# Performance work log

Measured on AMD Instinct MI355X. Metric: run time of the kernel, lower is better.

The kernel has to match this reference:

```python
import jax, jax.numpy as jnp
import numpy as np
from itertools import product

DIM = 384
HEADS = 8
DIM_HEAD = 64
INNER = HEADS * DIM_HEAD  # 512
KS = 3                    # kernel_size (attention window)
PAD = KS // 2
W_WIN = KS * KS           # 9
SCALE = DIM_HEAD ** -0.5


def setup_inputs() -> dict:
    key = jax.random.key(0)
    k1, k2, k3, k4, k5 = jax.random.split(key, 5)
    B, H, W = 4, 56, 56
    x = jax.random.normal(k1, (B, DIM, H, W), dtype=jnp.float32)
    # 1x1 conv weights stored as (out_ch, in_ch)
    Wq = jax.random.normal(k2, (INNER, DIM), dtype=jnp.float32) * (DIM ** -0.5)
    Wkv = jax.random.normal(k3, (2 * INNER, DIM), dtype=jnp.float32) * (DIM ** -0.5)
    Wo = jax.random.normal(k4, (DIM, INNER), dtype=jnp.float32) * (INNER ** -0.5)
    bo = jax.random.normal(k5, (DIM,), dtype=jnp.float32) * 0.01
    return {"x": x, "Wq": Wq, "Wkv": Wkv, "Wo": Wo, "bo": bo}


def _conv1x1(x, w):
    # x: (B,Cin,H,W), w: (Cout,Cin) -> (B,Cout,H,W)
    return jnp.einsum('bchw,oc->bohw', x, w)


def reference(x, Wq, Wkv, Wo, bo):
    B, C, H, W = x.shape
    q = _conv1x1(x, Wq)                       # (B, INNER, H, W)
    kv = _conv1x1(x, Wkv)                     # (B, 2*INNER, H, W)
    k, v = jnp.split(kv, 2, axis=1)
    # split channels heads-major, matching torch reshape (B, heads, dh, H, W)
    q = q.reshape(B, HEADS, DIM_HEAD, H, W)
    k = k.reshape(B, HEADS, DIM_HEAD, H, W)
    v = v.reshape(B, HEADS, DIM_HEAD, H, W)
    # zero-pad spatial dims (matches F.unfold zero padding: padded taps get logit 0)
    k_pad = jnp.pad(k, ((0, 0), (0, 0), (0, 0), (PAD, PAD), (PAD, PAD)))
    v_pad = jnp.pad(v, ((0, 0), (0, 0), (0, 0), (PAD, PAD), (PAD, PAD)))
    offsets = list(product(range(KS), range(KS)))  # row-major = unfold order
    # dots: (B, heads, H, W, w)
    dots = jnp.stack([
        jnp.einsum('bhdxy,bhdxy->bhxy', q, k_pad[:, :, :, i:i + H, j:j + W])
        for (i, j) in offsets
    ], axis=-1) * SCALE
    attn = jax.nn.softmax(dots, axis=-1)      # softmax over the 9-tap window
    # weighted sum of shifted v: (B, heads, dh, H, W)
    out = sum(
        attn[:, :, None, :, :, w_idx] * v_pad[:, :, :, i:i + H, j:j + W]
        for w_idx, (i, j) in enumerate(offsets)
    )
    out = out.reshape(B, INNER, H, W)
    return _conv1x1(out, Wo) + bo[None, :, None, None]
```

## Files before the change

### kernel.cpp

```cpp
#include <hip/hip_runtime.h>


#define HW 3136
#define WIMG 56
#define QKV_CH 1536
#define SCALE 0.125f
#define KSTR 72
#define NROWS 180
#define QKV_T 6422528

typedef __bf16 bf16x8_t __attribute__((ext_vector_type(8)));
typedef float f32x4_t __attribute__((ext_vector_type(4)));
typedef unsigned short ushort8 __attribute__((ext_vector_type(8)));

__device__ __forceinline__ float bf2f(unsigned short u) {
    return __uint_as_float(((unsigned int)u) << 16);
}
__device__ __forceinline__ unsigned short f2bf(float f) {
    unsigned int u = __float_as_uint(f);
    u += 0x7FFFu + ((u >> 16) & 1u);
    return (unsigned short)(u >> 16);
}

__device__ __forceinline__ void gll16(const unsigned short* g, unsigned short* l) {
    __builtin_amdgcn_global_load_lds(
        (const __attribute__((address_space(1))) unsigned int*)g,
        (__attribute__((address_space(3))) unsigned int*)l,
        16, 0, 0);
}

__global__ __launch_bounds__(256) void cvt_all(
    const float* __restrict__ x,
    const float* __restrict__ Wq, const float* __restrict__ Wkv,
    const float* __restrict__ Wo,
    unsigned short* __restrict__ xT,
    unsigned short* __restrict__ wT, unsigned short* __restrict__ wT3)
{
    __shared__ unsigned short Tl[64 * 36];
    const int bx = blockIdx.x;
    const int t = threadIdx.x;

    if (bx < 2400) {
        const int sblk = bx % 50;
        const int kblk = (bx / 50) % 12;
        const int b    = bx / 600;

        if (sblk == 49) {
            unsigned short* dst = xT + (((size_t)b * 25 + 24) * 12 + kblk) * 4096 + 2048;
            *reinterpret_cast<uint4*>(dst + t * 8) = (uint4){0, 0, 0, 0};
            return;
        }

        const float* xp = x + ((size_t)b * 384 + (size_t)kblk * 32) * HW + sblk * 64;
        const int c = t >> 3;
#pragma unroll
        for (int i = 0; i < 2; i++) {
            const int sc = (t & 7) + 8 * i;
            const float4 v = *reinterpret_cast<const float4*>(xp + (size_t)c * HW + sc * 4);
            const int s4 = sc * 4;
            Tl[(s4 + 0) * 36 + c] = f2bf(v.x);
            Tl[(s4 + 1) * 36 + c] = f2bf(v.y);
            Tl[(s4 + 2) * 36 + c] = f2bf(v.z);
            Tl[(s4 + 3) * 36 + c] = f2bf(v.w);
        }
        __syncthreads();

        const int row = t >> 2, gran = t & 3;
        const uint2 lo = *reinterpret_cast<const uint2*>(&Tl[row * 36 + gran * 8]);
        const uint2 hi = *reinterpret_cast<const uint2*>(&Tl[row * 36 + gran * 8 + 4]);
        uint4 o; o.x = lo.x; o.y = lo.y; o.z = hi.x; o.w = hi.y;
        unsigned short* dst = xT + (((size_t)b * 25 + (sblk >> 1)) * 12 + kblk) * 4096
                            + (sblk & 1) * 2048;
        *reinterpret_cast<uint4*>(dst + t * 8) = o;
        return;
    }

    const int i = (bx - 2400) * 256 + t;
    if (i < 73728) {
        const int g = i & 3;
        const int idx3 = i >> 2;
        const int o128 = idx3 & 127;
        const int rest = idx3 >> 7;
        const int kb = rest % 12, oblk = rest / 12;
        const int o = oblk * 128 + o128;
        const int k0 = kb * 32 + g * 8;
        const float* src = (o < 512) ? (Wq + (size_t)o * 384 + k0)
                                     : (Wkv + (size_t)(o - 512) * 384 + k0);
        const float4 v0 = *reinterpret_cast<const float4*>(src);
        const float4 v1 = *reinterpret_cast<const float4*>(src + 4);
        uint4 u;
        u.x = (unsigned int)f2bf(v0.x) | ((unsigned int)f2bf(v0.y) << 16);
        u.y = (unsigned int)f2bf(v0.z) | ((unsigned int)f2bf(v0.w) << 16);
        u.z = (unsigned int)f2bf(v1.x) | ((unsigned int)f2bf(v1.y) << 16);
        u.w = (unsigned int)f2bf(v1.z) | ((unsigned int)f2bf(v1.w) << 16);
        reinterpret_cast<uint4*>(wT)[i] = u;
    } else {
        const int j = i - 73728;
        const int g = j & 3;
        const int idx3 = j >> 2;
        const int o128 = idx3 & 127;
        const int rest = idx3 >> 7;
        const int kb = rest % 16, oblk = rest / 16;
        const int o = oblk * 128 + o128;
        const float* src = Wo + (size_t)o * 512 + kb * 32 + g * 8;
        const float4 v0 = *reinterpret_cast<const float4*>(src);
        const float4 v1 = *reinterpret_cast<const float4*>(src + 4);
        uint4 u;
        u.x = (unsigned int)f2bf(v0.x) | ((unsigned int)f2bf(v0.y) << 16);
        u.y = (unsigned int)f2bf(v0.z) | ((unsigned int)f2bf(v0.w) << 16);
        u.z = (unsigned int)f2bf(v1.x) | ((unsigned int)f2bf(v1.y) << 16);
        u.w = (unsigned int)f2bf(v1.z) | ((unsigned int)f2bf(v1.w) << 16);
        reinterpret_cast<uint4*>(wT3)[j] = u;
    }
}

__global__ __launch_bounds__(256) void gemm1(
    const unsigned short* __restrict__ xT,
    const unsigned short* __restrict__ wT,
    unsigned short* __restrict__ qkvT)
{
    __shared__ __align__(16) unsigned short A_lds[128 * 32];
    __shared__ __align__(16) unsigned short B_lds[128 * 32];

    const int sblk = blockIdx.x;
    const int oblk = blockIdx.y;
    const int b  = blockIdx.z;
    const int t  = threadIdx.x;
    const int lane = t & 63, w = t >> 6;
    const int quad = lane >> 4, mrow = lane & 15;
    const int wm = w >> 1, wn = w & 1;

    const unsigned short* wsrc = wT + ((size_t)oblk * 12) * 4096;
    const unsigned short* xsrc = xT + (((size_t)b * 25 + sblk) * 12) * 4096;

    f32x4_t acc[4][4];
#pragma unroll
    for (int m = 0; m < 4; m++)
#pragma unroll
        for (int n = 0; n < 4; n++) acc[m][n] = (f32x4_t){0.f, 0.f, 0.f, 0.f};

    for (int kb = 0; kb < 12; kb++) {
        __syncthreads();
        gll16(wsrc + (size_t)kb * 4096 + t * 8,        A_lds + t * 8);
        gll16(wsrc + (size_t)kb * 4096 + 2048 + t * 8, A_lds + 2048 + t * 8);
        gll16(xsrc + (size_t)kb * 4096 + t * 8,        B_lds + t * 8);
        gll16(xsrc + (size_t)kb * 4096 + 2048 + t * 8, B_lds + 2048 + t * 8);
        __syncthreads();

        bf16x8_t af[4], bf[4];
#pragma unroll
        for (int m = 0; m < 4; m++)
            af[m] = *reinterpret_cast<const bf16x8_t*>(&A_lds[(wm * 64 + m * 16 + mrow) * 32 + quad * 8]);
#pragma unroll
        for (int n = 0; n < 4; n++)
            bf[n] = *reinterpret_cast<const bf16x8_t*>(&B_lds[(wn * 64 + n * 16 + mrow) * 32 + quad * 8]);
#pragma unroll
        for (int m = 0; m < 4; m++)
#pragma unroll
            for (int n = 0; n < 4; n++)
                acc[m][n] = __builtin_amdgcn_mfma_f32_16x16x32_bf16(af[m], bf[n], acc[m][n], 0, 0, 0);
    }

    const int which = oblk >> 2;
    const int hq = (oblk & 3) * 2 + wm;
    const int s0 = sblk * 128 + wn * 64;
    unsigned short* outb = qkvT + (size_t)which * QKV_T
                         + ((size_t)(b * 8 + hq) * HW) * 64;
#pragma unroll
    for (int m = 0; m < 4; m++) {
        const int d0 = m * 16 + quad * 4;
#pragma unroll
        for (int n = 0; n < 4; n++) {
            const int ss = s0 + n * 16 + mrow;
            if (ss < HW) {
                uint2 u;
                u.x = (unsigned int)f2bf(acc[m][n][0]) | ((unsigned int)f2bf(acc[m][n][1]) << 16);
                u.y = (unsigned int)f2bf(acc[m][n][2]) | ((unsigned int)f2bf(acc[m][n][3]) << 16);
                *reinterpret_cast<uint2*>(outb + (size_t)ss * 64 + d0) = u;
            }
        }
    }
}

__global__ __launch_bounds__(256) void natt2(
    const unsigned short* __restrict__ qkvT,
    unsigned short* __restrict__ aoT)
{
    __shared__ __align__(16) unsigned short smem[2 * NROWS * KSTR];
    unsigned short* Kl = smem;
    unsigned short* Vl = smem + NROWS * KSTR;
    float* dred = reinterpret_cast<float*>(smem);

    const int t = threadIdx.x, lane = t & 63, w = t >> 6;
    const int sblk = blockIdx.x;
    const int s0 = sblk * 64;
    const int s  = s0 + lane;
    const int h  = blockIdx.y, b = blockIdx.z;
    const int y  = s / WIMG, xx = s % WIMG;

    const unsigned short* qg = qkvT + ((size_t)(b * 8 + h) * HW) * 64;
    const unsigned short* kg = qg + (size_t)QKV_T;
    const unsigned short* vg = qg + (size_t)(2 * QKV_T);

#pragma unroll
    for (int i = 0; i < 6; i++) {
        const int f = i * 256 + t;
        if (f < NROWS * 8) {
            const int row = f >> 3, c8 = f & 7;
            int srow = s0 - 59 + row;
            srow = min(max(srow, 0), HW - 1);
            const uint4 k4 = *reinterpret_cast<const uint4*>(kg + (size_t)srow * 64 + c8 * 8);
            const uint4 v4 = *reinterpret_cast<const uint4*>(vg + (size_t)srow * 64 + c8 * 8);
            *reinterpret_cast<uint4*>(&Kl[row * KSTR + c8 * 8]) = k4;
            *reinterpret_cast<uint4*>(&Vl[row * KSTR + c8 * 8]) = v4;
        }
    }

    int   roff[9];
    float msk[9];
#pragma unroll
    for (int ty = 0; ty < 3; ty++)
#pragma unroll
        for (int tx = 0; tx < 3; tx++) {
            const int tap = ty * 3 + tx;
            const int ny = y + ty - 1, nx = xx + tx - 1;
            const bool v = (ny >= 0) && (ny < WIMG) && (nx >= 0) && (nx < WIMG);
            roff[tap] = (v ? ((ty - 1) * WIMG + (tx - 1)) : 0) * KSTR;
            msk[tap]  = v ? 1.f : 0.f;
        }

    float qv[16];
    {
        const uint4 q0 = *reinterpret_cast<const uint4*>(qg + (size_t)s * 64 + w * 16);
        const uint4 q1 = *reinterpret_cast<const uint4*>(qg + (size_t)s * 64 + w * 16 + 8);
        qv[0] = bf2f((unsigned short)(q0.x & 0xffff)); qv[1] = bf2f((unsigned short)(q0.x >> 16));
        qv[2] = bf2f((unsigned short)(q0.y & 0xffff)); qv[3] = bf2f((unsigned short)(q0.y >> 16));
        qv[4] = bf2f((unsigned short)(q0.z & 0xffff)); qv[5] = bf2f((unsigned short)(q0.z >> 16));
        qv[6] = bf2f((unsigned short)(q0.w & 0xffff)); qv[7] = bf2f((unsigned short)(q0.w >> 16));
        qv[8]  = bf2f((unsigned short)(q1.x & 0xffff)); qv[9]  = bf2f((unsigned short)(q1.x >> 16));
        qv[10] = bf2f((unsigned short)(q1.y & 0xffff)); qv[11] = bf2f((unsigned short)(q1.y >> 16));
        qv[12] = bf2f((unsigned short)(q1.z & 0xffff)); qv[13] = bf2f((unsigned short)(q1.z >> 16));
        qv[14] = bf2f((unsigned short)(q1.w & 0xffff)); qv[15] = bf2f((unsigned short)(q1.w >> 16));
    }

    __syncthreads();

    const int rbase = (59 + lane) * KSTR + w * 16;

    float dots[9];
#pragma unroll
    for (int tp = 0; tp < 9; tp++) dots[tp] = 0.f;
#pragma unroll
    for (int hh = 0; hh < 2; hh++) {
#pragma unroll
        for (int tp = 0; tp < 9; tp++) {
            const ushort8 kk = *reinterpret_cast<const ushort8*>(&Kl[rbase + roff[tp] + hh * 8]);
#pragma unroll
            for (int j = 0; j < 8; j++)
                dots[tp] += qv[hh * 8 + j] * bf2f(kk[j]);
        }
    }

    __syncthreads();
#pragma unroll
    for (int tp = 0; tp < 9; tp++) dred[(tp * 4 + w) * 64 + lane] = dots[tp];
    __syncthreads();

    float mx = -1e30f, dt[9];
#pragma unroll
    for (int tp = 0; tp < 9; tp++) {
        const float sum = dred[(tp * 4 + 0) * 64 + lane] + dred[(tp * 4 + 1) * 64 + lane] +
                          dred[(tp * 4 + 2) * 64 + lane] + dred[(tp * 4 + 3) * 64 + lane];
        dt[tp] = msk[tp] * (sum * SCALE);
        mx = fmaxf(mx, dt[tp]);
    }
    float se = 0.f, w9[9];
#pragma unroll
    for (int tp = 0; tp < 9; tp++) { w9[tp] = __expf(dt[tp] - mx); se += w9[tp]; }
    const float inv = 1.f / se;
#pragma unroll
    for (int tp = 0; tp < 9; tp++) w9[tp] *= inv * msk[tp];

    float o[16];
#pragma unroll
    for (int dd = 0; dd < 16; dd++) o[dd] = 0.f;
#pragma unroll
    for (int hh = 0; hh < 2; hh++) {
        ushort8 vfr[9];
#pragma unroll
        for (int tp = 0; tp < 9; tp++)
            vfr[tp] = *reinterpret_cast<const ushort8*>(&Vl[rbase + roff[tp] + hh * 8]);
#pragma unroll
        for (int j = 0; j < 8; j++)
#pragma unroll
            for (int tp = 0; tp < 9; tp++)
                o[hh * 8 + j] += w9[tp] * bf2f(vfr[tp][j]);
    }

    __align__(16) unsigned short ov[16];
#pragma unroll
    for (int dd = 0; dd < 16; dd++) ov[dd] = f2bf(o[dd]);

    unsigned short* dst = aoT + (((size_t)(b * 49 + sblk)) * 16 + (h * 2 + (w >> 1))) * 2048
                        + lane * 32 + (w & 1) * 16;
    *reinterpret_cast<uint4*>(dst)     = *reinterpret_cast<const uint4*>(ov);
    *reinterpret_cast<uint4*>(dst + 8) = *reinterpret_cast<const uint4*>(ov + 8);
}

__global__ __launch_bounds__(256) void gemm3(
    const unsigned short* __restrict__ aoT,
    const unsigned short* __restrict__ wT3,
    const float* __restrict__ bias,
    float* __restrict__ out)
{
    __shared__ __align__(16) unsigned short A_lds[128 * 32];
    __shared__ __align__(16) unsigned short B_lds[64 * 32];

    const int sblk = blockIdx.x;
    const int oblk = blockIdx.y;
    const int b  = blockIdx.z;
    const int t  = threadIdx.x;
    const int lane = t & 63, w = t >> 6;
    const int quad = lane >> 4, mrow = lane & 15;
    const int wm = w >> 1, wn = w & 1;

    const unsigned short* asrc = wT3 + (size_t)oblk * 16 * 4096;
    const unsigned short* bsrc = aoT + ((size_t)(b * 49 + sblk)) * 16 * 2048;

    f32x4_t acc[4][2];
#pragma unroll
    for (int m = 0; m < 4; m++)
#pragma unroll
        for (int n = 0; n < 2; n++) acc[m][n] = (f32x4_t){0.f, 0.f, 0.f, 0.f};

    for (int kb = 0; kb < 16; kb++) {
        __syncthreads();
        gll16(asrc + (size_t)kb * 4096 + t * 8,        A_lds + t * 8);
        gll16(asrc + (size_t)kb * 4096 + 2048 + t * 8, A_lds + 2048 + t * 8);
        gll16(bsrc + (size_t)kb * 2048 + t * 8,        B_lds + t * 8);
        __syncthreads();

        bf16x8_t af[4], bf[2];
#pragma unroll
        for (int m = 0; m < 4; m++)
            af[m] = *reinterpret_cast<const bf16x8_t*>(&A_lds[(wm * 64 + m * 16 + mrow) * 32 + quad * 8]);
#pragma unroll
        for (int n = 0; n < 2; n++)
            bf[n] = *reinterpret_cast<const bf16x8_t*>(&B_lds[(wn * 32 + n * 16 + mrow) * 32 + quad * 8]);
#pragma unroll
        for (int m = 0; m < 4; m++)
#pragma unroll
            for (int n = 0; n < 2; n++)
                acc[m][n] = __builtin_amdgcn_mfma_f32_16x16x32_bf16(af[m], bf[n], acc[m][n], 0, 0, 0);
    }

    const int o0 = oblk * 128 + wm * 64;
    const int s0 = sblk * 64 + wn * 32;
    float* outb = out + (size_t)b * 384 * HW;
#pragma unroll
    for (int m = 0; m < 4; m++)
#pragma unroll
        for (int n = 0; n < 2; n++) {
            const int ss = s0 + n * 16 + mrow;
#pragma unroll
            for (int r = 0; r < 4; r++) {
                const int oo = o0 + m * 16 + quad * 4 + r;
                outb[(size_t)oo * HW + ss] = acc[m][n][r] + bias[oo];
            }
        }
}

extern "C" void kernel_launch(void* const* d_in, const int* in_sizes, int n_in,
                              void* d_out, int out_size, void* d_ws, size_t ws_size,
                              hipStream_t stream) {
    const float* x   = (const float*)d_in[0];
    const float* Wq  = (const float*)d_in[1];
    const float* Wkv = (const float*)d_in[2];
    const float* Wo  = (const float*)d_in[3];
    const float* bo  = (const float*)d_in[4];
    float* out = (float*)d_out;

    unsigned short* xT   = (unsigned short*)d_ws;
    unsigned short* wT   = xT + (size_t)4915200;
    unsigned short* wT3  = wT + (size_t)589824;
    unsigned short* qkvT = wT3 + (size_t)196608;
    unsigned short* aoT  = qkvT + (size_t)(3 * QKV_T);

    cvt_all<<<dim3(2784), 256, 0, stream>>>(x, Wq, Wkv, Wo, xT, wT, wT3);

    gemm1<<<dim3(25, 12, 4), 256, 0, stream>>>(xT, wT, qkvT);
    natt2<<<dim3(49, 8, 4), 256, 0, stream>>>(qkvT, aoT);
    gemm3<<<dim3(49, 3, 4), 256, 0, stream>>>(aoT, wT3, bo, out);
}
```

Baseline: 143.1 us.

## Widen neighborhood-attention tiles to 128 pixels and reuse one LDS buffer for K then V

Each natt2 block now covers 128 pixels instead of 64, with 2 threads per pixel splitting the head dim into 32-wide halves instead of 4 quarters. This cuts the halo overhead per pixel and the cross-thread dot reduction. K and V share one LDS buffer: V is loaded after the K dot products, which lowers LDS footprint but puts the V load on the critical path. The grid shrinks to 25x8x4 blocks, and the last block is masked at the image boundary.

Measured after the change: 141.1 us. No clear change (-1.4%).

```diff
diff --git a/kernel.cpp b/kernel.cpp
--- a/kernel.cpp
+++ b/kernel.cpp
@@ -6,7 +6,7 @@
 #define QKV_CH 1536
 #define SCALE 0.125f
 #define KSTR 72
-#define NROWS 180
+#define NROWS 242
 #define QKV_T 6422528
 
 typedef __bf16 bf16x8_t __attribute__((ext_vector_type(8)));
@@ -186,33 +186,32 @@
     const unsigned short* __restrict__ qkvT,
     unsigned short* __restrict__ aoT)
 {
-    __shared__ __align__(16) unsigned short smem[2 * NROWS * KSTR];
-    unsigned short* Kl = smem;
-    unsigned short* Vl = smem + NROWS * KSTR;
-    float* dred = reinterpret_cast<float*>(smem);
-
-    const int t = threadIdx.x, lane = t & 63, w = t >> 6;
+    __shared__ __align__(16) unsigned short KV[NROWS * KSTR];
+    __shared__ float dred[9 * 2 * 128];
+
+    const int t = threadIdx.x;
+    const int p  = t & 127;
+    const int dq = t >> 7;
     const int sblk = blockIdx.x;
-    const int s0 = sblk * 64;
-    const int s  = s0 + lane;
+    const int s0 = sblk * 128;
+    const int s  = s0 + p;
     const int h  = blockIdx.y, b = blockIdx.z;
-    const int y  = s / WIMG, xx = s % WIMG;
+    const int sc = min(s, HW - 1);
+    const int y  = sc / WIMG, xx = sc % WIMG;
 
     const unsigned short* qg = qkvT + ((size_t)(b * 8 + h) * HW) * 64;
     const unsigned short* kg = qg + (size_t)QKV_T;
     const unsigned short* vg = qg + (size_t)(2 * QKV_T);
 
 #pragma unroll
-    for (int i = 0; i < 6; i++) {
+    for (int i = 0; i < 8; i++) {
         const int f = i * 256 + t;
         if (f < NROWS * 8) {
             const int row = f >> 3, c8 = f & 7;
-            int srow = s0 - 59 + row;
+            int srow = s0 - 57 + row;
             srow = min(max(srow, 0), HW - 1);
             const uint4 k4 = *reinterpret_cast<const uint4*>(kg + (size_t)srow * 64 + c8 * 8);
-            const uint4 v4 = *reinterpret_cast<const uint4*>(vg + (size_t)srow * 64 + c8 * 8);
-            *reinterpret_cast<uint4*>(&Kl[row * KSTR + c8 * 8]) = k4;
-            *reinterpret_cast<uint4*>(&Vl[row * KSTR + c8 * 8]) = v4;
+            *reinterpret_cast<uint4*>(&KV[row * KSTR + c8 * 8]) = k4;
         }
     }
 
@@ -229,48 +228,56 @@
             msk[tap]  = v ? 1.f : 0.f;
         }
 
-    float qv[16];
-    {
-        const uint4 q0 = *reinterpret_cast<const uint4*>(qg + (size_t)s * 64 + w * 16);
-        const uint4 q1 = *reinterpret_cast<const uint4*>(qg + (size_t)s * 64 + w * 16 + 8);
-        qv[0] = bf2f((unsigned short)(q0.x & 0xffff)); qv[1] = bf2f((unsigned short)(q0.x >> 16));
-        qv[2] = bf2f((unsigned short)(q0.y & 0xffff)); qv[3] = bf2f((unsigned short)(q0.y >> 16));
-        qv[4] = bf2f((unsigned short)(q0.z & 0xffff)); qv[5] = bf2f((unsigned short)(q0.z >> 16));
-        qv[6] = bf2f((unsigned short)(q0.w & 0xffff)); qv[7] = bf2f((unsigned short)(q0.w >> 16));
-        qv[8]  = bf2f((unsigned short)(q1.x & 0xffff)); qv[9]  = bf2f((unsigned short)(q1.x >> 16));
-        qv[10] = bf2f((unsigned short)(q1.y & 0xffff)); qv[11] = bf2f((unsigned short)(q1.y >> 16));
-        qv[12] = bf2f((unsigned short)(q1.z & 0xffff)); qv[13] = bf2f((unsigned short)(q1.z >> 16));
-        qv[14] = bf2f((unsigned short)(q1.w & 0xffff)); qv[15] = bf2f((unsigned short)(q1.w >> 16));
+    float qv[32];
+#pragma unroll
+    for (int c = 0; c < 4; c++) {
+        const uint4 q4 = *reinterpret_cast<const uint4*>(qg + (size_t)sc * 64 + dq * 32 + c * 8);
+        qv[c*8+0] = bf2f((unsigned short)(q4.x & 0xffff)); qv[c*8+1] = bf2f((unsigned short)(q4.x >> 16));
+        qv[c*8+2] = bf2f((unsigned short)(q4.y & 0xffff)); qv[c*8+3] = bf2f((unsigned short)(q4.y >> 16));
+        qv[c*8+4] = bf2f((unsigned short)(q4.z & 0xffff)); qv[c*8+5] = bf2f((unsigned short)(q4.z >> 16));
+        qv[c*8+6] = bf2f((unsigned short)(q4.w & 0xffff)); qv[c*8+7] = bf2f((unsigned short)(q4.w >> 16));
     }
 
     __syncthreads();
 
-    const int rbase = (59 + lane) * KSTR + w * 16;
+    const int rbase = (57 + p) * KSTR + dq * 32;
 
     float dots[9];
 #pragma unroll
     for (int tp = 0; tp < 9; tp++) dots[tp] = 0.f;
 #pragma unroll
-    for (int hh = 0; hh < 2; hh++) {
+    for (int ch = 0; ch < 4; ch++) {
 #pragma unroll
         for (int tp = 0; tp < 9; tp++) {
-            const ushort8 kk = *reinterpret_cast<const ushort8*>(&Kl[rbase + roff[tp] + hh * 8]);
+            const ushort8 kk = *reinterpret_cast<const ushort8*>(&KV[rbase + roff[tp] + ch * 8]);
 #pragma unroll
             for (int j = 0; j < 8; j++)
-                dots[tp] += qv[hh * 8 + j] * bf2f(kk[j]);
+                dots[tp] += qv[ch * 8 + j] * bf2f(kk[j]);
         }
     }
 
     __syncthreads();
-#pragma unroll
-    for (int tp = 0; tp < 9; tp++) dred[(tp * 4 + w) * 64 + lane] = dots[tp];
+
+#pragma unroll
+    for (int tp = 0; tp < 9; tp++) dred[(tp * 2 + dq) * 128 + p] = dots[tp];
+#pragma unroll
+    for (int i = 0; i < 8; i++) {
+        const int f = i * 256 + t;
+        if (f < NROWS * 8) {
+            const int row = f >> 3, c8 = f & 7;
+            int srow = s0 - 57 + row;
+            srow = min(max(srow, 0), HW - 1);
+            const uint4 v4 = *reinterpret_cast<const uint4*>(vg + (size_t)srow * 64 + c8 * 8);
+            *reinterpret_cast<uint4*>(&KV[row * KSTR + c8 * 8]) = v4;
+        }
+    }
+
     __syncthreads();
 
     float mx = -1e30f, dt[9];
 #pragma unroll
     for (int tp = 0; tp < 9; tp++) {
-        const float sum = dred[(tp * 4 + 0) * 64 + lane] + dred[(tp * 4 + 1) * 64 + lane] +
-                          dred[(tp * 4 + 2) * 64 + lane] + dred[(tp * 4 + 3) * 64 + lane];
+        const float sum = dred[(tp * 2 + 0) * 128 + p] + dred[(tp * 2 + 1) * 128 + p];
         dt[tp] = msk[tp] * (sum * SCALE);
         mx = fmaxf(mx, dt[tp]);
     }
@@ -281,30 +288,33 @@
 #pragma unroll
     for (int tp = 0; tp < 9; tp++) w9[tp] *= inv * msk[tp];
 
-    float o[16];
-#pragma unroll
-    for (int dd = 0; dd < 16; dd++) o[dd] = 0.f;
-#pragma unroll
-    for (int hh = 0; hh < 2; hh++) {
+    float o[32];
+#pragma unroll
+    for (int dd = 0; dd < 32; dd++) o[dd] = 0.f;
+#pragma unroll
+    for (int ch = 0; ch < 4; ch++) {
         ushort8 vfr[9];
 #pragma unroll
         for (int tp = 0; tp < 9; tp++)
-            vfr[tp] = *reinterpret_cast<const ushort8*>(&Vl[rbase + roff[tp] + hh * 8]);
+            vfr[tp] = *reinterpret_cast<const ushort8*>(&KV[rbase + roff[tp] + ch * 8]);
 #pragma unroll
         for (int j = 0; j < 8; j++)
 #pragma unroll
             for (int tp = 0; tp < 9; tp++)
-                o[hh * 8 + j] += w9[tp] * bf2f(vfr[tp][j]);
-    }
-
-    __align__(16) unsigned short ov[16];
-#pragma unroll
-    for (int dd = 0; dd < 16; dd++) ov[dd] = f2bf(o[dd]);
-
-    unsigned short* dst = aoT + (((size_t)(b * 49 + sblk)) * 16 + (h * 2 + (w >> 1))) * 2048
-                        + lane * 32 + (w & 1) * 16;
-    *reinterpret_cast<uint4*>(dst)     = *reinterpret_cast<const uint4*>(ov);
-    *reinterpret_cast<uint4*>(dst + 8) = *reinterpret_cast<const uint4*>(ov + 8);
+                o[ch * 8 + j] += w9[tp] * bf2f(vfr[tp][j]);
+    }
+
+    if (s < HW) {
+        __align__(16) unsigned short ov[32];
+#pragma unroll
+        for (int dd = 0; dd < 32; dd++) ov[dd] = f2bf(o[dd]);
+        unsigned short* dst = aoT + (((size_t)(b * 49 + (s >> 6))) * 16 + (h * 2 + dq)) * 2048
+                            + (s & 63) * 32;
+        *reinterpret_cast<uint4*>(dst)      = *reinterpret_cast<const uint4*>(ov);
+        *reinterpret_cast<uint4*>(dst + 8)  = *reinterpret_cast<const uint4*>(ov + 8);
+        *reinterpret_cast<uint4*>(dst + 16) = *reinterpret_cast<const uint4*>(ov + 16);
+        *reinterpret_cast<uint4*>(dst + 24) = *reinterpret_cast<const uint4*>(ov + 24);
+    }
 }
 
 __global__ __launch_bounds__(256) void gemm3(
@@ -389,6 +399,6 @@
     cvt_all<<<dim3(2784), 256, 0, stream>>>(x, Wq, Wkv, Wo, xT, wT, wT3);
 
     gemm1<<<dim3(25, 12, 4), 256, 0, stream>>>(xT, wT, qkvT);
-    natt2<<<dim3(49, 8, 4), 256, 0, stream>>>(qkvT, aoT);
+    natt2<<<dim3(25, 8, 4), 256, 0, stream>>>(qkvT, aoT);
     gemm3<<<dim3(49, 3, 4), 256, 0, stream>>>(aoT, wT3, bo, out);
 }
```
